# Kernel optimization log

Hardware: AMD Instinct MI355X
Metric: run time of the kernel (lower is better)

The kernel has to match this reference:

```python
import jax, jax.numpy as jnp
import numpy as np

N_NODES = 10000
NEG_SLOPE = 0.2  # PyG GATv2Conv default


def gatv2(x, src, dst, Wl, bl, Wr, br, att, bias, n_nodes):
    """Single-head GATv2Conv (PyG defaults: heads=1, concat=True, self-loops added by caller)."""
    xl = x @ Wl + bl            # [N, dout] message source transform (lin_l)
    xr = x @ Wr + br            # [N, dout] target transform (lin_r)
    h = jax.nn.leaky_relu(xl[src] + xr[dst], NEG_SLOPE)   # [E, dout]
    e = h @ att                                            # [E] attention logits
    m = jax.ops.segment_max(e, dst, num_segments=n_nodes)  # per-target max
    ex = jnp.exp(e - m[dst])
    s = jax.ops.segment_sum(ex, dst, num_segments=n_nodes)
    alpha = ex / s[dst]                                    # segment softmax over incoming edges
    out = jax.ops.segment_sum(alpha[:, None] * xl[src], dst, num_segments=n_nodes)
    return out + bias


def _glorot(key, shape, scale=0.05):
    return jax.random.normal(key, shape, dtype=jnp.float32) * scale


def setup_inputs() -> dict:
    key = jax.random.key(0)
    ks = jax.random.split(key, 20)
    d_in, d0, d1 = 1000, 256, 128
    E = 320000
    x = jax.random.normal(ks[0], (N_NODES, d_in), dtype=jnp.float32)
    edge_index = jax.random.randint(ks[1], (2, E), 0, N_NODES, dtype=jnp.int64)
    return {
        "x": x,
        "edge_index": edge_index,
        # proj_in: d_in -> 256
        "Wpi": _glorot(ks[2], (d_in, d0)), "bpi": jnp.zeros((d0,), jnp.float32),
        # enc GATv2Conv 256 -> 128
        "Wl1": _glorot(ks[3], (d0, d1)), "bl1": jnp.zeros((d1,), jnp.float32),
        "Wr1": _glorot(ks[4], (d0, d1)), "br1": jnp.zeros((d1,), jnp.float32),
        "att1": _glorot(ks[5], (d1,)), "bias1": jnp.zeros((d1,), jnp.float32),
        # dec GATv2Conv 128 -> 256
        "Wl2": _glorot(ks[6], (d1, d0)), "bl2": jnp.zeros((d0,), jnp.float32),
        "Wr2": _glorot(ks[7], (d1, d0)), "br2": jnp.zeros((d0,), jnp.float32),
        "att2": _glorot(ks[8], (d0,)), "bias2": jnp.zeros((d0,), jnp.float32),
        # proj_out: 256 -> d_in
        "Wpo": _glorot(ks[9], (d0, d_in)), "bpo": jnp.zeros((d_in,), jnp.float32),
    }


def reference(x, edge_index, Wpi, bpi, Wl1, bl1, Wr1, br1, att1, bias1,
              Wl2, bl2, Wr2, br2, att2, bias2, Wpo, bpo):
    n = x.shape[0]
    # add self-loops (PyG GATv2Conv default add_self_loops=True)
    loops = jnp.arange(n, dtype=edge_index.dtype)
    src = jnp.concatenate([edge_index[0], loops])
    dst = jnp.concatenate([edge_index[1], loops])
    h = x @ Wpi + bpi
    z = gatv2(h, src, dst, Wl1, bl1, Wr1, br1, att1, bias1, n)
    d = gatv2(z, src, dst, Wl2, bl2, Wr2, br2, att2, bias2, n)
    x_hat = d @ Wpo + bpo
    return (x_hat, z)
```

## Files before the change

### kernel.cpp

```cpp
#include <hip/hip_runtime.h>
#include <math.h>

#define N_NODES 10000
#define MPAD    10112
#define D_IN    1000
#define KPAD_IN 1024
#define D0      256
#define D1      128
#define NPAD_OUT 1024
#define NEG_SLOPE 0.2f

typedef __attribute__((ext_vector_type(8))) short short8;
typedef __attribute__((ext_vector_type(4))) float f32x4;

__device__ __forceinline__ ushort f2bf(float f) {
  union { float f; unsigned u; } c; c.f = f;
  unsigned r = c.u + 0x7FFF + ((c.u >> 16) & 1);
  return (ushort)(r >> 16);
}
__device__ __forceinline__ float bf2f(ushort b) {
  union { unsigned u; float f; } c; c.u = ((unsigned)b) << 16;
  return c.f;
}


__global__ void count_kernel(const int* __restrict__ idx, int E, int n, int* __restrict__ counts) {
  int k = blockIdx.x * blockDim.x + threadIdx.x;
  int tot = E + n;
  if (k >= tot) return;
  int dst = (k < E) ? idx[E + k] : (k - E);
  atomicAdd(&counts[dst], 1);
}

__global__ void scan_kernel(const int* __restrict__ counts, int* __restrict__ offsets,
                            int* __restrict__ cursors, int n) {
  __shared__ int tsum[1024];
  int tid = threadIdx.x;
  int per = (n + 1023) / 1024;
  int start = tid * per;
  int end = start + per; if (end > n) end = n;
  int s = 0;
  for (int i = start; i < end; i++) s += counts[i];
  tsum[tid] = s;
  __syncthreads();
  for (int off = 1; off < 1024; off <<= 1) {
    int v = (tid >= off) ? tsum[tid - off] : 0;
    __syncthreads();
    if (tid >= off) tsum[tid] += v;
    __syncthreads();
  }
  int run = (tid == 0) ? 0 : tsum[tid - 1];
  for (int i = start; i < end; i++) {
    offsets[i] = run; cursors[i] = run;
    run += counts[i];
  }
  if (tid == 1023) offsets[n] = tsum[1023];
}

__global__ void scatter_kernel(const int* __restrict__ idx, int E, int n,
                               int* __restrict__ cursors, int* __restrict__ srcs) {
  int k = blockIdx.x * blockDim.x + threadIdx.x;
  int tot = E + n;
  if (k >= tot) return;
  int src, dst;
  if (k < E) { src = idx[k]; dst = idx[E + k]; }
  else       { src = k - E;  dst = src; }
  int pos = atomicAdd(&cursors[dst], 1);
  srcs[pos] = src;
}


__global__ void conv_x_kernel(const float* __restrict__ x, ushort* __restrict__ xb) {
  int idx = blockIdx.x * blockDim.x + threadIdx.x;
  int r = idx >> 8, k4 = (idx & 255) * 4;
  ushort4 o = {0, 0, 0, 0};
  if (r < N_NODES && k4 < D_IN) {
    float4 v = *(const float4*)(x + (size_t)r * D_IN + k4);
    o.x = f2bf(v.x); o.y = f2bf(v.y); o.z = f2bf(v.z); o.w = f2bf(v.w);
  }
  *(ushort4*)(xb + (size_t)idx * 4) = o;
}

#define T_WPI   (256 * 1024)
#define T_W1    (256 * 256)
#define T_W2    (512 * 128)
#define T_WPO   (1024 * 256)
#define OFF_W1  T_WPI
#define OFF_W2  (OFF_W1 + T_W1)
#define OFF_WPO (OFF_W2 + T_W2)
#define OFF_B   (OFF_WPO + T_WPO)
#define T_ALL   (OFF_B + 768)

__global__ void wprep_all(const float* __restrict__ Wpi,
                          const float* __restrict__ Wl1, const float* __restrict__ Wr1,
                          const float* __restrict__ Wl2, const float* __restrict__ Wr2,
                          const float* __restrict__ Wpo,
                          const float* __restrict__ bl1, const float* __restrict__ br1,
                          const float* __restrict__ bl2, const float* __restrict__ br2,
                          ushort* __restrict__ Wpi_t, ushort* __restrict__ W1cat,
                          ushort* __restrict__ W2cat, ushort* __restrict__ Wpo_t,
                          float* __restrict__ bcat1, float* __restrict__ bcat2) {
  int idx = blockIdx.x * 256 + threadIdx.x;
  if (idx >= T_ALL) return;
  if (idx < OFF_W1) {
    int n = idx >> 10, k = idx & 1023;
    Wpi_t[idx] = f2bf((k < 1000) ? Wpi[(size_t)k * 256 + n] : 0.f);
  } else if (idx < OFF_W2) {
    int q = idx - OFF_W1, n = q >> 8, k = q & 255;
    float v = (n < 128) ? Wl1[k * 128 + n] : Wr1[k * 128 + (n - 128)];
    W1cat[q] = f2bf(v);
  } else if (idx < OFF_WPO) {
    int q = idx - OFF_W2, n = q >> 7, k = q & 127;
    float v = (n < 256) ? Wl2[k * 256 + n] : Wr2[k * 256 + (n - 256)];
    W2cat[q] = f2bf(v);
  } else if (idx < OFF_B) {
    int q = idx - OFF_WPO, n = q >> 8, k = q & 255;
    Wpo_t[q] = f2bf((n < 1000) ? Wpo[(size_t)k * 1000 + n] : 0.f);
  } else {
    int q = idx - OFF_B;
    if (q < 128)      bcat1[q] = bl1[q];
    else if (q < 256) bcat1[q] = br1[q - 128];
    else if (q < 512) bcat2[q - 256] = bl2[q - 256];
    else              bcat2[q - 256] = br2[q - 512];
  }
}


template<int MODE>
__launch_bounds__(256)
__global__ void gemm_mfma(const ushort* __restrict__ A, int lda,
                          const ushort* __restrict__ Bt, int ldb,
                          const float* __restrict__ bias,
                          float* __restrict__ Cf, ushort* __restrict__ Cb, int ldp,
                          int M_valid, int N_valid, int K) {
  constexpr int BK = 32;
  __shared__ ushort As[128 * BK];
  __shared__ ushort Bs[128 * BK];
  const int tid  = threadIdx.x;
  const int lane = tid & 63, wave = tid >> 6;
  const int wr = wave >> 1, wc = wave & 1;
  const int bm = blockIdx.y * 128, bn = blockIdx.x * 128;
  const int r16 = lane & 15, kb = lane >> 4;

  f32x4 acc[4][4] = {};

  const int srow = tid >> 2;
  const int scol = (tid & 3) * 8;
  const ushort* Ag0 = A  + (size_t)(bm + srow) * lda + scol;
  const ushort* Ag1 = A  + (size_t)(bm + 64 + srow) * lda + scol;
  const ushort* Bg0 = Bt + (size_t)(bn + srow) * ldb + scol;
  const ushort* Bg1 = Bt + (size_t)(bn + 64 + srow) * ldb + scol;

  for (int k0 = 0; k0 < K; k0 += BK) {
    __builtin_amdgcn_global_load_lds((const __attribute__((address_space(1))) void*)(Ag0 + k0),
                                     (__attribute__((address_space(3))) void*)(As + tid * 8), 16, 0, 0);
    __builtin_amdgcn_global_load_lds((const __attribute__((address_space(1))) void*)(Ag1 + k0),
                                     (__attribute__((address_space(3))) void*)(As + 2048 + tid * 8), 16, 0, 0);
    __builtin_amdgcn_global_load_lds((const __attribute__((address_space(1))) void*)(Bg0 + k0),
                                     (__attribute__((address_space(3))) void*)(Bs + tid * 8), 16, 0, 0);
    __builtin_amdgcn_global_load_lds((const __attribute__((address_space(1))) void*)(Bg1 + k0),
                                     (__attribute__((address_space(3))) void*)(Bs + 2048 + tid * 8), 16, 0, 0);
    __syncthreads();

    short8 af[4], bfr[4];
    #pragma unroll
    for (int mi = 0; mi < 4; mi++)
      af[mi] = *(const short8*)(As + ((wr * 64 + mi * 16 + r16) * BK + kb * 8));
    #pragma unroll
    for (int ni = 0; ni < 4; ni++)
      bfr[ni] = *(const short8*)(Bs + ((wc * 64 + ni * 16 + r16) * BK + kb * 8));
    #pragma unroll
    for (int mi = 0; mi < 4; mi++)
      #pragma unroll
      for (int ni = 0; ni < 4; ni++)
        acc[mi][ni] = __builtin_amdgcn_mfma_f32_16x16x32_bf16(af[mi], bfr[ni], acc[mi][ni], 0, 0, 0);
    __syncthreads();
  }

  #pragma unroll
  for (int mi = 0; mi < 4; mi++) {
    const int row = bm + wr * 64 + mi * 16 + (lane >> 4) * 4;
    #pragma unroll
    for (int ni = 0; ni < 4; ni++) {
      const int col = bn + wc * 64 + ni * 16 + r16;
      const float bv = (col < N_valid) ? bias[col] : 0.f;
      #pragma unroll
      for (int r = 0; r < 4; r++) {
        const int gr = row + r;
        const float val = acc[mi][ni][r] + bv;
        if constexpr (MODE == 0) {
          if (gr < M_valid && col < N_valid) Cf[(size_t)gr * ldp + col] = val;
        } else if constexpr (MODE == 1) {
          Cb[(size_t)gr * ldp + col] = f2bf(gr < M_valid ? val : 0.f);
        } else {
          if (col < ldp) Cb[(size_t)gr * ldp + col] = f2bf(val);
          else           Cf[(size_t)gr * ldp + (col - ldp)] = val;
        }
      }
    }
  }
}


template<int D>
__launch_bounds__(256)
__global__ void gat_fused(const ushort* __restrict__ xlb, const float* __restrict__ xrf,
                          const float* __restrict__ att, const float* __restrict__ bias,
                          const int* __restrict__ offsets, const int* __restrict__ srcs,
                          float* __restrict__ out_f32, ushort* __restrict__ out_bf16,
                          int n_valid, int Etot) {
  constexpr int EPL = D / 64;
  const int tid  = threadIdx.x;
  const int lane = tid & 63;
  const int wave = tid >> 6;
  const int v    = blockIdx.x * 4 + wave;
  const int d0   = lane * EPL;

  if (v >= n_valid) {
    if (out_bf16) {
      if constexpr (EPL == 4) *(ushort4*)(out_bf16 + (size_t)v * D + d0) = ushort4{0, 0, 0, 0};
      else                    *(ushort2*)(out_bf16 + (size_t)v * D + d0) = ushort2{0, 0};
    }
    return;
  }

  float rv[EPL], av[EPL], acc[EPL];
  #pragma unroll
  for (int d = 0; d < EPL; d++) {
    rv[d]  = xrf[(size_t)v * D + d0 + d];
    av[d]  = att[d0 + d];
    acc[d] = 0.f;
  }

  const int beg = offsets[v], end = offsets[v + 1];
  float m = -INFINITY, s = 0.f;

  ushort xnxt[EPL];
  {
    const int u0 = srcs[beg];
    if constexpr (EPL == 4) *(ushort4*)xnxt = *(const ushort4*)(xlb + (size_t)u0 * D + d0);
    else                    *(ushort2*)xnxt = *(const ushort2*)(xlb + (size_t)u0 * D + d0);
  }

  for (int k = beg; k < end; k++) {
    ushort xcur[EPL];
    #pragma unroll
    for (int d = 0; d < EPL; d++) xcur[d] = xnxt[d];

    const int kn = (k + 1 < Etot) ? k + 1 : k;
    const int un = srcs[kn];
    if constexpr (EPL == 4) *(ushort4*)xnxt = *(const ushort4*)(xlb + (size_t)un * D + d0);
    else                    *(ushort2*)xnxt = *(const ushort2*)(xlb + (size_t)un * D + d0);

    float xv[EPL], p = 0.f;
    #pragma unroll
    for (int d = 0; d < EPL; d++) {
      xv[d] = bf2f(xcur[d]);
      float t = xv[d] + rv[d];
      t = fmaxf(t, NEG_SLOPE * t);
      p = fmaf(t, av[d], p);
    }
    #pragma unroll
    for (int off = 32; off > 0; off >>= 1) p += __shfl_xor(p, off);

    const float m2   = fmaxf(m, p);
    const float cold = __expf(m - m2);
    const float w    = __expf(p - m2);
    s = s * cold + w;
    #pragma unroll
    for (int d = 0; d < EPL; d++) acc[d] = fmaf(acc[d], cold, w * xv[d]);
    m = m2;
  }

  const float inv = 1.f / s;
  float o[EPL];
  #pragma unroll
  for (int d = 0; d < EPL; d++) o[d] = fmaf(acc[d], inv, bias[d0 + d]);

  if (out_f32) {
    if constexpr (EPL == 4) *(float4*)(out_f32 + (size_t)v * D + d0) = float4{o[0], o[1], o[2], o[3]};
    else                    *(float2*)(out_f32 + (size_t)v * D + d0) = float2{o[0], o[1]};
  }
  if (out_bf16) {
    if constexpr (EPL == 4)
      *(ushort4*)(out_bf16 + (size_t)v * D + d0) = ushort4{f2bf(o[0]), f2bf(o[1]), f2bf(o[2]), f2bf(o[3])};
    else
      *(ushort2*)(out_bf16 + (size_t)v * D + d0) = ushort2{f2bf(o[0]), f2bf(o[1])};
  }
}


extern "C" void kernel_launch(void* const* d_in, const int* in_sizes, int n_in,
                              void* d_out, int out_size, void* d_ws, size_t ws_size,
                              hipStream_t stream) {
  const float* x     = (const float*)d_in[0];
  const int*   eidx  = (const int*)d_in[1];
  const float* Wpi   = (const float*)d_in[2];
  const float* bpi   = (const float*)d_in[3];
  const float* Wl1   = (const float*)d_in[4];
  const float* bl1   = (const float*)d_in[5];
  const float* Wr1   = (const float*)d_in[6];
  const float* br1   = (const float*)d_in[7];
  const float* att1  = (const float*)d_in[8];
  const float* bias1 = (const float*)d_in[9];
  const float* Wl2   = (const float*)d_in[10];
  const float* bl2   = (const float*)d_in[11];
  const float* Wr2   = (const float*)d_in[12];
  const float* br2   = (const float*)d_in[13];
  const float* att2  = (const float*)d_in[14];
  const float* bias2 = (const float*)d_in[15];
  const float* Wpo   = (const float*)d_in[16];
  const float* bpo   = (const float*)d_in[17];

  const int E    = in_sizes[1] / 2;
  const int n    = N_NODES;
  const int Etot = E + n;

  float* out_xhat = (float*)d_out;
  float* out_z    = (float*)d_out + (size_t)N_NODES * D_IN;

  char* wp = (char*)d_ws;
  auto alloc = [&](size_t bytes) { char* p = wp; wp += (bytes + 255) & ~(size_t)255; return p; };
  char* regionA = (char*)alloc((size_t)MPAD * KPAD_IN * 2);
  ushort* hb_db = (ushort*)alloc((size_t)MPAD * D0 * 2);
  ushort* zb    = (ushort*)alloc((size_t)MPAD * D1 * 2);
  int* counts  = (int*)alloc((size_t)n * 4);
  int* offsets = (int*)alloc((size_t)(n + 1) * 4);
  int* cursors = (int*)alloc((size_t)n * 4);
  int* srcs    = (int*)alloc((size_t)Etot * 4);
  ushort* Wpi_t = (ushort*)alloc((size_t)T_WPI * 2);
  ushort* W1cat = (ushort*)alloc((size_t)T_W1 * 2);
  ushort* W2cat = (ushort*)alloc((size_t)T_W2 * 2);
  ushort* Wpo_t = (ushort*)alloc((size_t)T_WPO * 2);
  float*  bcat1 = (float*)alloc(256 * 4);
  float*  bcat2 = (float*)alloc(512 * 4);

  ushort* xb   = (ushort*)regionA;
  float*  xr1f = (float*)regionA;
  ushort* xl1b = (ushort*)(regionA + 8 * 1024 * 1024);
  float*  xr2f = (float*)regionA;
  ushort* xl2b = (ushort*)(regionA + 12 * 1024 * 1024);
  ushort* hb   = hb_db;
  ushort* db   = hb_db;

  hipMemsetAsync(counts, 0, (size_t)n * 4, stream);
  const int tb = 256;
  count_kernel<<<(Etot + tb - 1) / tb, tb, 0, stream>>>(eidx, E, n, counts);
  scan_kernel<<<1, 1024, 0, stream>>>(counts, offsets, cursors, n);
  scatter_kernel<<<(Etot + tb - 1) / tb, tb, 0, stream>>>(eidx, E, n, cursors, srcs);

  conv_x_kernel<<<MPAD, 256, 0, stream>>>(x, xb);
  wprep_all<<<(T_ALL + 255) / 256, 256, 0, stream>>>(
      Wpi, Wl1, Wr1, Wl2, Wr2, Wpo, bl1, br1, bl2, br2,
      Wpi_t, W1cat, W2cat, Wpo_t, bcat1, bcat2);

  gemm_mfma<1><<<dim3(D0 / 128, MPAD / 128), 256, 0, stream>>>(
      xb, KPAD_IN, Wpi_t, KPAD_IN, bpi, nullptr, hb, D0, N_NODES, D0, KPAD_IN);
  gemm_mfma<2><<<dim3(256 / 128, MPAD / 128), 256, 0, stream>>>(
      hb, D0, W1cat, D0, bcat1, xr1f, xl1b, D1, N_NODES, 256, D0);
  gat_fused<D1><<<MPAD / 4, 256, 0, stream>>>(xl1b, xr1f, att1, bias1,
                                              offsets, srcs, out_z, zb, N_NODES, Etot);
  gemm_mfma<2><<<dim3(512 / 128, MPAD / 128), 256, 0, stream>>>(
      zb, D1, W2cat, D1, bcat2, xr2f, xl2b, D0, N_NODES, 512, D1);
  gat_fused<D0><<<MPAD / 4, 256, 0, stream>>>(xl2b, xr2f, att2, bias2,
                                              offsets, srcs, nullptr, db, N_NODES, Etot);
  gemm_mfma<0><<<dim3(NPAD_OUT / 128, MPAD / 128), 256, 0, stream>>>(
      db, D0, Wpo_t, D0, bpo, out_xhat, nullptr, D_IN, N_NODES, D_IN, D0);
}
```

Before: 346.0 us.

## Split each node's edge loop across four waves and merge softmax partials in LDS

The GAT aggregation kernel now assigns one block per target node instead of one wave per node. Each of the four waves processes every fourth incoming edge with its own online softmax state, and the partial maxima, sums and accumulators are combined through shared memory. This shortens the serial per-edge dependency chain (~33 edges per node) and adds memory-level parallelism for the gathers. The cost is four times as many blocks, two block barriers, and LDS traffic for the reduction.

```diff
diff --git a/kernel.cpp b/kernel.cpp
--- a/kernel.cpp
+++ b/kernel.cpp
@@ -208,21 +208,22 @@
                           const float* __restrict__ att, const float* __restrict__ bias,
                           const int* __restrict__ offsets, const int* __restrict__ srcs,
                           float* __restrict__ out_f32, ushort* __restrict__ out_bf16,
-                          int n_valid, int Etot) {
+                          int n_valid) {
   constexpr int EPL = D / 64;
+  const int v    = blockIdx.x;
   const int tid  = threadIdx.x;
   const int lane = tid & 63;
   const int wave = tid >> 6;
-  const int v    = blockIdx.x * 4 + wave;
   const int d0   = lane * EPL;
 
   if (v >= n_valid) {
-    if (out_bf16) {
-      if constexpr (EPL == 4) *(ushort4*)(out_bf16 + (size_t)v * D + d0) = ushort4{0, 0, 0, 0};
-      else                    *(ushort2*)(out_bf16 + (size_t)v * D + d0) = ushort2{0, 0};
-    }
+    if (out_bf16 && tid < D) out_bf16[(size_t)v * D + tid] = 0;
     return;
   }
+
+  __shared__ float m_s[4];
+  __shared__ float s_s[4];
+  __shared__ float buf[4][D];
 
   float rv[EPL], av[EPL], acc[EPL];
   #pragma unroll
@@ -235,22 +236,25 @@
   const int beg = offsets[v], end = offsets[v + 1];
   float m = -INFINITY, s = 0.f;
 
+  int k = beg + wave;
   ushort xnxt[EPL];
-  {
-    const int u0 = srcs[beg];
+  if (k < end) {
+    const int u0 = srcs[k];
     if constexpr (EPL == 4) *(ushort4*)xnxt = *(const ushort4*)(xlb + (size_t)u0 * D + d0);
     else                    *(ushort2*)xnxt = *(const ushort2*)(xlb + (size_t)u0 * D + d0);
   }
 
-  for (int k = beg; k < end; k++) {
+  for (; k < end; k += 4) {
     ushort xcur[EPL];
     #pragma unroll
     for (int d = 0; d < EPL; d++) xcur[d] = xnxt[d];
 
-    const int kn = (k + 1 < Etot) ? k + 1 : k;
-    const int un = srcs[kn];
-    if constexpr (EPL == 4) *(ushort4*)xnxt = *(const ushort4*)(xlb + (size_t)un * D + d0);
-    else                    *(ushort2*)xnxt = *(const ushort2*)(xlb + (size_t)un * D + d0);
+    const int kn = k + 4;
+    if (kn < end) {
+      const int un = srcs[kn];
+      if constexpr (EPL == 4) *(ushort4*)xnxt = *(const ushort4*)(xlb + (size_t)un * D + d0);
+      else                    *(ushort2*)xnxt = *(const ushort2*)(xlb + (size_t)un * D + d0);
+    }
 
     float xv[EPL], p = 0.f;
     #pragma unroll
@@ -272,20 +276,20 @@
     m = m2;
   }
 
-  const float inv = 1.f / s;
-  float o[EPL];
+  if (lane == 0) m_s[wave] = m;
+  __syncthreads();
+  const float M = fmaxf(fmaxf(m_s[0], m_s[1]), fmaxf(m_s[2], m_s[3]));
+  const float c = __expf(m - M);
+  if (lane == 0) s_s[wave] = s * c;
   #pragma unroll
-  for (int d = 0; d < EPL; d++) o[d] = fmaf(acc[d], inv, bias[d0 + d]);
-
-  if (out_f32) {
-    if constexpr (EPL == 4) *(float4*)(out_f32 + (size_t)v * D + d0) = float4{o[0], o[1], o[2], o[3]};
-    else                    *(float2*)(out_f32 + (size_t)v * D + d0) = float2{o[0], o[1]};
-  }
-  if (out_bf16) {
-    if constexpr (EPL == 4)
-      *(ushort4*)(out_bf16 + (size_t)v * D + d0) = ushort4{f2bf(o[0]), f2bf(o[1]), f2bf(o[2]), f2bf(o[3])};
-    else
-      *(ushort2*)(out_bf16 + (size_t)v * D + d0) = ushort2{f2bf(o[0]), f2bf(o[1])};
+  for (int d = 0; d < EPL; d++) buf[wave][d0 + d] = acc[d] * c;
+  __syncthreads();
+
+  if (tid < D) {
+    const float stot = s_s[0] + s_s[1] + s_s[2] + s_s[3];
+    const float val = (buf[0][tid] + buf[1][tid] + buf[2][tid] + buf[3][tid]) / stot + bias[tid];
+    if (out_f32)  out_f32[(size_t)v * D + tid] = val;
+    if (out_bf16) out_bf16[(size_t)v * D + tid] = f2bf(val);
   }
 }
 
@@ -358,12 +362,12 @@
       xb, KPAD_IN, Wpi_t, KPAD_IN, bpi, nullptr, hb, D0, N_NODES, D0, KPAD_IN);
   gemm_mfma<2><<<dim3(256 / 128, MPAD / 128), 256, 0, stream>>>(
       hb, D0, W1cat, D0, bcat1, xr1f, xl1b, D1, N_NODES, 256, D0);
-  gat_fused<D1><<<MPAD / 4, 256, 0, stream>>>(xl1b, xr1f, att1, bias1,
-                                              offsets, srcs, out_z, zb, N_NODES, Etot);
+  gat_fused<D1><<<MPAD, 256, 0, stream>>>(xl1b, xr1f, att1, bias1,
+                                          offsets, srcs, out_z, zb, N_NODES);
   gemm_mfma<2><<<dim3(512 / 128, MPAD / 128), 256, 0, stream>>>(
       zb, D1, W2cat, D1, bcat2, xr2f, xl2b, D0, N_NODES, 512, D1);
-  gat_fused<D0><<<MPAD / 4, 256, 0, stream>>>(xl2b, xr2f, att2, bias2,
-                                              offsets, srcs, nullptr, db, N_NODES, Etot);
+  gat_fused<D0><<<MPAD, 256, 0, stream>>>(xl2b, xr2f, att2, bias2,
+                                          offsets, srcs, nullptr, db, N_NODES);
   gemm_mfma<0><<<dim3(NPAD_OUT / 128, MPAD / 128), 256, 0, stream>>>(
       db, D0, Wpo_t, D0, bpo, out_xhat, nullptr, D_IN, N_NODES, D_IN, D0);
 }
```

Result: no change. 347.9 us (+0.6%).
